# Optimization experiments

Hardware: AMD Instinct MI355X
Metric: run time of the kernel (lower is better)

## Reference

```python
import jax, jax.numpy as jnp
import numpy as np

KH, KW = 2, 2  # kernel_shape: stride-2 zero-insertion unpool

def setup_inputs() -> dict:
    key = jax.random.key(0)
    x = jax.random.normal(key, (32, 112, 112, 64), dtype=jnp.float32)
    return {"x": x}

def reference(x) -> jnp.ndarray:
    # Equivalent to conv2d_transpose with identity-in-top-left kernel and
    # stride (KH, KW): each input element goes to the top-left of a KHxKW
    # zero block. Output shape: [B, H*KH, W*KW, C].
    b, h, w, c = x.shape
    out = jnp.zeros((b, h * KH, w * KW, c), dtype=x.dtype)
    out = out.at[:, ::KH, ::KW, :].set(x)
    return out
```

## Files before the change

### kernel.cpp

```cpp
#include <hip/hip_runtime.h>


__global__ __launch_bounds__(256) void unpool_kernel(
    const float4* __restrict__ x, float4* __restrict__ out) {
    const int j  = blockIdx.x * 256 + threadIdx.x;
    const int oh = blockIdx.y;
    const int b  = blockIdx.z;
    const int c4 = j & 15;
    const int ow = j >> 4;

    float4 v = make_float4(0.f, 0.f, 0.f, 0.f);
    if (((oh | ow) & 1) == 0) {
        v = x[((b * 112 + (oh >> 1)) * 112 + (ow >> 1)) * 16 + c4];
    }
    out[(b * 224 + oh) * 3584 + j] = v;
}

extern "C" void kernel_launch(void* const* d_in, const int* in_sizes, int n_in,
                              void* d_out, int out_size, void* d_ws, size_t ws_size,
                              hipStream_t stream) {
    const float4* x = (const float4*)d_in[0];
    float4* out = (float4*)d_out;
    dim3 grid(14, 224, 32);
    dim3 block(256);
    unpool_kernel<<<grid, block, 0, stream>>>(x, out);
}
```

Measured before the change: 457.5 us.

## Process output row pairs per block with nontemporal loads and stores

Each block now handles one input row and writes both the even output row (data plus zeros) and the odd all-zero row, with each thread covering two float4 positions. Loads and stores use nontemporal builtins to bypass cache retention for the streaming data. This cuts the grid to a quarter of the blocks and removes the row-parity branch, in exchange for more work per thread and less parallelism per block.

```diff
diff --git a/kernel.cpp b/kernel.cpp
--- a/kernel.cpp
+++ b/kernel.cpp
@@ -1,27 +1,42 @@
 #include <hip/hip_runtime.h>
 
+typedef float f4 __attribute__((ext_vector_type(4)));
 
 __global__ __launch_bounds__(256) void unpool_kernel(
-    const float4* __restrict__ x, float4* __restrict__ out) {
-    const int j  = blockIdx.x * 256 + threadIdx.x;
-    const int oh = blockIdx.y;
-    const int b  = blockIdx.z;
-    const int c4 = j & 15;
-    const int ow = j >> 4;
+    const f4* __restrict__ x, f4* __restrict__ out) {
+    const int tid = threadIdx.x;
+    const int j0  = blockIdx.x * 512 + tid;
+    const int j1  = j0 + 256;
+    const int h   = blockIdx.y;
+    const int b   = blockIdx.z;
 
-    float4 v = make_float4(0.f, 0.f, 0.f, 0.f);
-    if (((oh | ow) & 1) == 0) {
-        v = x[((b * 112 + (oh >> 1)) * 112 + (ow >> 1)) * 16 + c4];
+    const int c4_0 = j0 & 15, ow0 = j0 >> 4;
+    const int c4_1 = j1 & 15, ow1 = j1 >> 4;
+
+    const f4 z = (f4){0.f, 0.f, 0.f, 0.f};
+
+    f4* orow_e = out + (size_t)(b * 224 + 2 * h) * 3584;
+    f4* orow_o = orow_e + 3584;
+
+    __builtin_nontemporal_store(z, &orow_o[j0]);
+    __builtin_nontemporal_store(z, &orow_o[j1]);
+
+    f4 v0 = z, v1 = z;
+    if ((ow0 & 1) == 0) {
+        const f4* xrow = x + (size_t)(b * 112 + h) * (112 * 16);
+        v0 = __builtin_nontemporal_load(&xrow[(ow0 >> 1) * 16 + c4_0]);
+        v1 = __builtin_nontemporal_load(&xrow[(ow1 >> 1) * 16 + c4_1]);
     }
-    out[(b * 224 + oh) * 3584 + j] = v;
+    __builtin_nontemporal_store(v0, &orow_e[j0]);
+    __builtin_nontemporal_store(v1, &orow_e[j1]);
 }
 
 extern "C" void kernel_launch(void* const* d_in, const int* in_sizes, int n_in,
                               void* d_out, int out_size, void* d_ws, size_t ws_size,
                               hipStream_t stream) {
-    const float4* x = (const float4*)d_in[0];
-    float4* out = (float4*)d_out;
-    dim3 grid(14, 224, 32);
+    const f4* x = (const f4*)d_in[0];
+    f4* out = (f4*)d_out;
+    dim3 grid(7, 112, 32);
     dim3 block(256);
     unpool_kernel<<<grid, block, 0, stream>>>(x, out);
 }
```

New measurement: 452.3 us. Within noise of the previous version (-1.2%).
